# Kernel tuning notes

Hardware: AMD Instinct MI355X
Metric: run time of the kernel (lower is better)

Reference implementation:

```python
import jax, jax.numpy as jnp
import numpy as np

B, T, D, U = 32, 2048, 512, 512

def setup_inputs() -> dict:
    key = jax.random.key(0)
    ks = jax.random.split(key, 7)
    s = 1.0 / np.sqrt(D)
    return {
        "query": jax.random.normal(ks[0], (B, D), jnp.float32),
        "values": jax.random.normal(ks[1], (B, T, D), jnp.float32),
        "W1": jax.random.normal(ks[2], (D, U), jnp.float32) * s,
        "b1": jnp.zeros((U,), jnp.float32),
        "W2": jax.random.normal(ks[3], (D, U), jnp.float32) * s,
        "b2": jnp.zeros((U,), jnp.float32),
        "V": jax.random.normal(ks[4], (U, 1), jnp.float32) * (1.0 / np.sqrt(U)),
        "bV": jnp.zeros((1,), jnp.float32),
    }

def reference(query, values, W1, b1, W2, b2, V, bV):
    # values: [B,T,D], query: [B,D]
    proj_v = jnp.einsum('btd,du->btu', values, W1) + b1          # [B,T,U]
    proj_q = (query @ W2 + b2)[:, None, :]                        # [B,1,U]
    score = jnp.tanh(proj_v + proj_q) @ V + bV                    # [B,T,1]
    attention_weights = jax.nn.softmax(score, axis=1)             # [B,T,1]
    context_vector = jnp.sum(attention_weights * values, axis=1)  # [B,D]
    return (context_vector, attention_weights)
```

## Files before the change

### kernel.cpp

```cpp
#include <hip/hip_runtime.h>
#include <hip/hip_bf16.h>
#include <math.h>

#define BB 32
#define TT 2048
#define DD 512
#define UU 512

typedef __attribute__((ext_vector_type(8))) short short8v;
typedef __attribute__((ext_vector_type(4))) float floatx4;
typedef __attribute__((ext_vector_type(8))) unsigned short ushort8v;
typedef __attribute__((ext_vector_type(4))) unsigned short ushort4v;

static __device__ inline unsigned short f2bf(float f) {
  __hip_bfloat16 h = __float2bfloat16(f);
  return *reinterpret_cast<unsigned short*>(&h);
}

static __device__ inline float bf2f(unsigned short u) {
  union { unsigned int i; float f; } x;
  x.i = ((unsigned int)u) << 16;
  return x.f;
}

static __device__ inline float fast_tanh(float x) {
  x = fminf(fmaxf(x, -15.f), 15.f);
  float e2 = __expf(2.f * x);
  return (e2 - 1.f) * __builtin_amdgcn_rcpf(e2 + 1.f);
}

__global__ __launch_bounds__(256) void prep_kernel(
    const float* __restrict__ W1, unsigned short* __restrict__ w1a,
    const float* __restrict__ query, const float* __restrict__ W2,
    const float* __restrict__ b2, const float* __restrict__ b1,
    float* __restrict__ qb) {
  __shared__ float Wf[32][132];
  const int tid = threadIdx.x;
  if (blockIdx.x < 64) {
    const int kt = blockIdx.x & 15, uc = blockIdx.x >> 4;
    {
      const int k = tid >> 3;
      const int u16 = (tid & 7) * 16;
      const float* src = W1 + (size_t)(kt * 32 + k) * UU + uc * 128 + u16;
      #pragma unroll
      for (int q = 0; q < 4; ++q) {
        const float4 v = *(const float4*)(src + q * 4);
        Wf[k][u16 + q * 4 + 0] = v.x;
        Wf[k][u16 + q * 4 + 1] = v.y;
        Wf[k][u16 + q * 4 + 2] = v.z;
        Wf[k][u16 + q * 4 + 3] = v.w;
      }
    }
    __syncthreads();
    unsigned short* dst = w1a + (size_t)kt * 16384;
    #pragma unroll
    for (int s = 0; s < 2; ++s) {
      const int c = s * 256 + tid;
      const int kg = c >> 7;
      const int u = c & 127;
      ushort8v o;
      #pragma unroll
      for (int e = 0; e < 8; ++e) o[e] = f2bf(Wf[kg * 8 + e][u]);
      *(ushort8v*)(dst + ((size_t)kg * 512 + uc * 128 + u) * 8) = o;
    }
  } else {
    const int bidx = blockIdx.x - 64;
    const int b = bidx >> 1;
    const int u = (bidx & 1) * 256 + tid;
    float acc = b2[u] + b1[u];
    const float* q = query + b * DD;
    #pragma unroll 16
    for (int d = 0; d < DD; ++d) acc += q[d] * W2[(size_t)d * UU + u];
    qb[b * UU + u] = acc;
  }
}

#define SBM 64

__global__ __launch_bounds__(512, 4) void score_fused_kernel(
    const float* __restrict__ values, const unsigned short* __restrict__ w1a,
    const float* __restrict__ qb, const float* __restrict__ V,
    float* __restrict__ score, float* __restrict__ o_part,
    float* __restrict__ l_part) {
  __shared__ __align__(16) unsigned short Bp[2][8][4][SBM][8];
  __shared__ float qv_lds[512];
  __shared__ float vv_lds[512];
  __shared__ float part[8][SBM];
  __shared__ float sw[SBM];
  __shared__ float opart[4][512];

  const int tid = threadIdx.x;
  const int row0 = blockIdx.x * SBM;
  const int b = row0 >> 11;
  const int lane = tid & 63;
  const int wid = tid >> 6;
  const int wu = wid * 64;
  const int fr = lane & 15;
  const int kg = lane >> 4;

  qv_lds[tid] = qb[b * UU + tid];
  vv_lds[tid] = V[tid];

  const int sm = tid >> 3;
  const int sj = tid & 7;
  const float* bsrc = values + (size_t)(row0 + sm) * DD + sj * 4;
  const int bofs = (sj >> 1) * (SBM * 8) + sm * 8 + (sj & 1) * 4;

  {
    float4 r0[8];
    #pragma unroll
    for (int q = 0; q < 8; ++q)
      r0[q] = *(const float4*)(bsrc + (size_t)q * 32);
    #pragma unroll
    for (int q = 0; q < 8; ++q) {
      ushort4v o = {f2bf(r0[q].x), f2bf(r0[q].y), f2bf(r0[q].z), f2bf(r0[q].w)};
      *(ushort4v*)(&Bp[0][q][0][0][0] + bofs) = o;
    }
  }

  const size_t aofs = (size_t)(kg * 512 + wu + fr) * 8;
  short8v af[3][4];
  #pragma unroll
  for (int ju = 0; ju < 4; ++ju) {
    af[0][ju] = *(const short8v*)(w1a + aofs + (size_t)ju * 128);
    af[1][ju] = *(const short8v*)(w1a + 16384 + aofs + (size_t)ju * 128);
  }

  __syncthreads();

  float4 r1[8];
  #pragma unroll
  for (int q = 0; q < 8; ++q)
    r1[q] = *(const float4*)(bsrc + (size_t)(8 + q) * 32);

  floatx4 acc[4][4] = {};

  #pragma unroll
  for (int t = 0; t < 16; ++t) {
    if (t == 8) {
      #pragma unroll
      for (int q = 0; q < 8; ++q) {
        ushort4v o = {f2bf(r1[q].x), f2bf(r1[q].y), f2bf(r1[q].z), f2bf(r1[q].w)};
        *(ushort4v*)(&Bp[1][q][0][0][0] + bofs) = o;
      }
      __syncthreads();
    }

    if (t + 2 < 16) {
      #pragma unroll
      for (int ju = 0; ju < 4; ++ju)
        af[(t + 2) % 3][ju] =
            *(const short8v*)(w1a + (size_t)(t + 2) * 16384 + aofs + (size_t)ju * 128);
    }

    #pragma unroll
    for (int jm = 0; jm < 4; ++jm) {
      const short8v bfv = *(const short8v*)&Bp[t >> 3][t & 7][kg][jm * 16 + fr][0];
      #pragma unroll
      for (int ju = 0; ju < 4; ++ju)
        acc[ju][jm] = __builtin_amdgcn_mfma_f32_16x16x32_bf16(af[t % 3][ju], bfv, acc[ju][jm], 0, 0, 0);
    }
  }

  float pm[4] = {0.f, 0.f, 0.f, 0.f};
  #pragma unroll
  for (int ju = 0; ju < 4; ++ju) {
    const float4 qv = *(const float4*)&qv_lds[wu + ju * 16 + kg * 4];
    const float4 vv = *(const float4*)&vv_lds[wu + ju * 16 + kg * 4];
    const float qa[4] = {qv.x, qv.y, qv.z, qv.w};
    const float va[4] = {vv.x, vv.y, vv.z, vv.w};
    #pragma unroll
    for (int jm = 0; jm < 4; ++jm)
      #pragma unroll
      for (int reg = 0; reg < 4; ++reg)
        pm[jm] += fast_tanh(acc[ju][jm][reg] + qa[reg]) * va[reg];
  }
  #pragma unroll
  for (int jm = 0; jm < 4; ++jm) {
    pm[jm] += __shfl_xor(pm[jm], 16, 64);
    pm[jm] += __shfl_xor(pm[jm], 32, 64);
  }
  if (lane < 16) {
    #pragma unroll
    for (int jm = 0; jm < 4; ++jm) part[wid][jm * 16 + lane] = pm[jm];
  }
  __syncthreads();
  if (tid < SBM) {
    float s = 0.f;
    #pragma unroll
    for (int w = 0; w < 8; ++w) s += part[w][tid];
    score[row0 + tid] = s;
    sw[tid] = __expf(s);
  }
  __syncthreads();

  {
    const int g = tid >> 7;
    const int dq = tid & 127;
    const int half = dq >> 6;
    const int ktl = (dq >> 3) & 7;
    const int kgl = (dq >> 1) & 3;
    const int e = (dq & 1) * 4;
    float4 o4 = {0.f, 0.f, 0.f, 0.f};
    #pragma unroll
    for (int r = 0; r < 16; ++r) {
      const int m = g * 16 + r;
      const float w = sw[m];
      const ushort4v v4 = *(const ushort4v*)&Bp[half][ktl][kgl][m][e];
      o4.x += w * bf2f(v4[0]);
      o4.y += w * bf2f(v4[1]);
      o4.z += w * bf2f(v4[2]);
      o4.w += w * bf2f(v4[3]);
    }
    *(float4*)&opart[g][dq * 4] = o4;
  }
  if (wid == 0) {
    float lv = sw[lane];
    #pragma unroll
    for (int m = 1; m < 64; m <<= 1) lv += __shfl_xor(lv, m, 64);
    if (lane == 0) l_part[blockIdx.x] = lv;
  }
  __syncthreads();
  {
    const int d = tid;
    o_part[(size_t)blockIdx.x * DD + d] =
        opart[0][d] + opart[1][d] + opart[2][d] + opart[3][d];
  }
}

__global__ __launch_bounds__(128) void finish_kernel(
    const float* __restrict__ o_part, const float* __restrict__ l_part,
    const float* __restrict__ score, float* __restrict__ ctx,
    float* __restrict__ attn) {
  if (blockIdx.x < 32) {
    const int b = blockIdx.x;
    const int d0 = threadIdx.x * 4;
    float Ls = 0.f;
    #pragma unroll 8
    for (int c = 0; c < 32; ++c) Ls += l_part[b * 32 + c];
    const float inv = 1.f / Ls;
    float4 a = {0.f, 0.f, 0.f, 0.f};
    #pragma unroll 8
    for (int c = 0; c < 32; ++c) {
      const float4 p = *(const float4*)(o_part + (size_t)(b * 32 + c) * DD + d0);
      a.x += p.x; a.y += p.y; a.z += p.z; a.w += p.w;
    }
    a.x *= inv; a.y *= inv; a.z *= inv; a.w *= inv;
    *(float4*)(ctx + (size_t)b * DD + d0) = a;
  } else {
    const int c = blockIdx.x - 32;
    const int b = c >> 1;
    float Ls = 0.f;
    #pragma unroll 8
    for (int q = 0; q < 32; ++q) Ls += l_part[b * 32 + q];
    const float inv = 1.f / Ls;
    const int base = c * 1024 + threadIdx.x;
    #pragma unroll
    for (int q = 0; q < 8; ++q) {
      const int i = base + q * 128;
      attn[i] = __expf(score[i]) * inv;
    }
  }
}

extern "C" void kernel_launch(void* const* d_in, const int* in_sizes, int n_in,
                              void* d_out, int out_size, void* d_ws, size_t ws_size,
                              hipStream_t stream) {
  const float* query  = (const float*)d_in[0];
  const float* values = (const float*)d_in[1];
  const float* W1     = (const float*)d_in[2];
  const float* b1     = (const float*)d_in[3];
  const float* W2     = (const float*)d_in[4];
  const float* b2     = (const float*)d_in[5];
  const float* V      = (const float*)d_in[6];

  float* ctx  = (float*)d_out;
  float* attn = (float*)d_out + BB * DD;

  float* qb           = (float*)d_ws;
  float* score        = qb + BB * UU;
  unsigned short* w1a = (unsigned short*)(score + BB * TT);
  float* o_part       = (float*)(w1a + (size_t)UU * DD);
  float* l_part       = o_part + (size_t)1024 * DD;

  prep_kernel<<<128, 256, 0, stream>>>(W1, w1a, query, W2, b2, b1, qb);

  score_fused_kernel<<<(BB * TT) / SBM, 512, 0, stream>>>(
      values, w1a, qb, V, score, o_part, l_part);

  finish_kernel<<<96, 128, 0, stream>>>(o_part, l_part, score, ctx, attn);
}
```

Before: 80.31 us.

## Split second-half values staging into two chunks and re-read fp32 values for context

```diff
diff --git a/kernel.cpp b/kernel.cpp
--- a/kernel.cpp
+++ b/kernel.cpp
@@ -15,12 +15,6 @@
 static __device__ inline unsigned short f2bf(float f) {
   __hip_bfloat16 h = __float2bfloat16(f);
   return *reinterpret_cast<unsigned short*>(&h);
-}
-
-static __device__ inline float bf2f(unsigned short u) {
-  union { unsigned int i; float f; } x;
-  x.i = ((unsigned int)u) << 16;
-  return x.f;
 }
 
 static __device__ inline float fast_tanh(float x) {
@@ -119,38 +113,48 @@
   }
 
   const size_t aofs = (size_t)(kg * 512 + wu + fr) * 8;
-  short8v af[3][4];
-  #pragma unroll
-  for (int ju = 0; ju < 4; ++ju) {
+  short8v af[2][4];
+  #pragma unroll
+  for (int ju = 0; ju < 4; ++ju)
     af[0][ju] = *(const short8v*)(w1a + aofs + (size_t)ju * 128);
-    af[1][ju] = *(const short8v*)(w1a + 16384 + aofs + (size_t)ju * 128);
-  }
-
-  __syncthreads();
-
-  float4 r1[8];
-  #pragma unroll
-  for (int q = 0; q < 8; ++q)
+
+  __syncthreads();
+
+  float4 r1[4];
+  #pragma unroll
+  for (int q = 0; q < 4; ++q)
     r1[q] = *(const float4*)(bsrc + (size_t)(8 + q) * 32);
 
   floatx4 acc[4][4] = {};
 
   #pragma unroll
   for (int t = 0; t < 16; ++t) {
-    if (t == 8) {
-      #pragma unroll
-      for (int q = 0; q < 8; ++q) {
+    const int cur = t & 1;
+
+    if (t == 3) {
+      #pragma unroll
+      for (int q = 0; q < 4; ++q) {
         ushort4v o = {f2bf(r1[q].x), f2bf(r1[q].y), f2bf(r1[q].z), f2bf(r1[q].w)};
         *(ushort4v*)(&Bp[1][q][0][0][0] + bofs) = o;
       }
-      __syncthreads();
-    }
-
-    if (t + 2 < 16) {
+      #pragma unroll
+      for (int q = 0; q < 4; ++q)
+        r1[q] = *(const float4*)(bsrc + (size_t)(12 + q) * 32);
+    }
+    if (t == 7) {
+      #pragma unroll
+      for (int q = 0; q < 4; ++q) {
+        ushort4v o = {f2bf(r1[q].x), f2bf(r1[q].y), f2bf(r1[q].z), f2bf(r1[q].w)};
+        *(ushort4v*)(&Bp[1][4 + q][0][0][0] + bofs) = o;
+      }
+    }
+    if (t == 8) __syncthreads();
+
+    if (t + 1 < 16) {
       #pragma unroll
       for (int ju = 0; ju < 4; ++ju)
-        af[(t + 2) % 3][ju] =
-            *(const short8v*)(w1a + (size_t)(t + 2) * 16384 + aofs + (size_t)ju * 128);
+        af[cur ^ 1][ju] =
+            *(const short8v*)(w1a + (size_t)(t + 1) * 16384 + aofs + (size_t)ju * 128);
     }
 
     #pragma unroll
@@ -158,7 +162,7 @@
       const short8v bfv = *(const short8v*)&Bp[t >> 3][t & 7][kg][jm * 16 + fr][0];
       #pragma unroll
       for (int ju = 0; ju < 4; ++ju)
-        acc[ju][jm] = __builtin_amdgcn_mfma_f32_16x16x32_bf16(af[t % 3][ju], bfv, acc[ju][jm], 0, 0, 0);
+        acc[ju][jm] = __builtin_amdgcn_mfma_f32_16x16x32_bf16(af[cur][ju], bfv, acc[ju][jm], 0, 0, 0);
     }
   }
 
@@ -197,20 +201,13 @@
   {
     const int g = tid >> 7;
     const int dq = tid & 127;
-    const int half = dq >> 6;
-    const int ktl = (dq >> 3) & 7;
-    const int kgl = (dq >> 1) & 3;
-    const int e = (dq & 1) * 4;
+    const float* vrow = values + (size_t)(row0 + g * 16) * DD + dq * 4;
     float4 o4 = {0.f, 0.f, 0.f, 0.f};
     #pragma unroll
     for (int r = 0; r < 16; ++r) {
-      const int m = g * 16 + r;
-      const float w = sw[m];
-      const ushort4v v4 = *(const ushort4v*)&Bp[half][ktl][kgl][m][e];
-      o4.x += w * bf2f(v4[0]);
-      o4.y += w * bf2f(v4[1]);
-      o4.z += w * bf2f(v4[2]);
-      o4.w += w * bf2f(v4[3]);
+      const float w = sw[g * 16 + r];
+      const float4 v = *(const float4*)(vrow + (size_t)r * DD);
+      o4.x += w * v.x; o4.y += w * v.y; o4.z += w * v.z; o4.w += w * v.w;
     }
     *(float4*)&opart[g][dq * 4] = o4;
   }
```

New measurement: 93.88 us. 1.17x slower.
